# Optimization experiments

Hardware: AMD Instinct MI355X
Metric: run time of the kernel (lower is better)

## Reference

```python
import jax, jax.numpy as jnp
import numpy as np

D = 512        # input_dim
T = 64         # n_trees
DEPTH = 3
NI = 2 ** DEPTH - 1   # 7 internal nodes
NL = 2 ** DEPTH       # 8 leaves
PPT = NI * D + NI + NL * 2   # params per tree
TOT = PPT * T + T            # + tree_weights
HID = 64


def setup_inputs() -> dict:
    key = jax.random.key(0)
    ks = jax.random.split(key, 10)
    w = lambda k, s: jax.random.normal(k, s, jnp.float32) * 0.05  # xavier-ish small gain
    return {
        "X_train": jax.random.normal(ks[0], (8192, D), jnp.float32),
        "X_test": jax.random.normal(ks[1], (32768, D), jnp.float32),
        "y_train": jax.random.randint(ks[2], (8192,), 0, 2, jnp.int64),
        "W1": w(ks[3], (HID, D)), "b1": jnp.zeros(HID), "g1": jnp.ones(HID), "be1": jnp.zeros(HID),
        "W2": w(ks[4], (HID, HID)), "b2": jnp.zeros(HID),
        "H1": w(ks[5], (2 * HID, HID)), "hb1": jnp.zeros(2 * HID),
        "g2": jnp.ones(2 * HID), "be2": jnp.zeros(2 * HID),
        "H2": w(ks[6], (2 * HID, 2 * HID)), "hb2": jnp.zeros(2 * HID),
        "H3": w(ks[7], (TOT, 2 * HID)), "hb3": jnp.zeros(TOT),
    }


def _ln(x, g, b, eps=1e-5):
    m = x.mean(-1, keepdims=True)
    v = ((x - m) ** 2).mean(-1, keepdims=True)
    return (x - m) / jnp.sqrt(v + eps) * g + b


def reference(X_train, X_test, y_train, W1, b1, g1, be1, W2, b2,
              H1, hb1, g2, be2, H2, hb2, H3, hb3):
    # --- hypernet: data encoder + param generator (Dropout is eval=identity) ---
    h = jax.nn.relu(_ln(X_train @ W1.T + b1, g1, be1))
    h = jax.nn.relu(h @ W2.T + b2)
    c = h.mean(axis=0)                              # [HID] context
    u = jax.nn.relu(_ln(c @ H1.T + hb1, g2, be2))
    u = jax.nn.relu(u @ H2.T + hb2)
    params = u @ H3.T + hb3                         # [TOT]

    # --- parse per-tree params (sequential layout) ---
    rows = params[: T * PPT].reshape(T, PPT)
    sw = rows[:, : NI * D].reshape(T, NI, D)        # split weights
    sb = rows[:, NI * D: NI * D + NI]               # split bias [T, NI]
    ll = rows[:, NI * D + NI:].reshape(T, NL, 2)    # leaf logits
    tw = params[T * PPT:]                           # tree weights [T]

    # --- soft decision trees, all trees/nodes batched ---
    # sigmoid split prob for every (sample, tree, internal node); temperature=1
    p = jax.nn.sigmoid(jnp.einsum('bd,tnd->btn', X_test, sw) + sb[None])  # [B,T,NI]
    B = X_test.shape[0]
    lp = jnp.ones((B, T, 1), X_test.dtype)
    for d in range(DEPTH):                          # unrolled fixed-depth traversal
        s = 2 ** d - 1                              # heap offset of level d
        pd = p[:, :, s: s + 2 ** d]                 # [B,T,2^d]
        lp = jnp.stack([lp * (1 - pd), lp * pd], axis=-1).reshape(B, T, 2 ** (d + 1))
    # original code adds leaf contributions twice (main loop + cleanup loop)
    lp = lp * 2.0                                   # [B,T,NL]

    leaf_dist = jax.nn.softmax(ll, axis=-1)         # [T,NL,2]
    out_t = jnp.einsum('btl,tlc->btc', lp, leaf_dist)
    w = jax.nn.softmax(tw, axis=0)                  # [T]
    return jnp.einsum('btc,t->bc', out_t, w)        # [B,2]
```

## Files before the change

kernel.cpp:

```cpp
#include <hip/hip_runtime.h>
#include <hip/hip_bf16.h>

#define DD 512
#define HIDN 64
#define NTREE 64
#define NIN 7
#define PPTC 3607
#define TOTP 230912
#define SWROWS 448

typedef __attribute__((ext_vector_type(8))) short bf16x8;
typedef __attribute__((ext_vector_type(4))) float f32x4;
typedef __attribute__((ext_vector_type(8))) _Float16 h16x8;

__device__ __forceinline__ unsigned short f2bf(float f) {
  unsigned u = __float_as_uint(f);
  unsigned r = (u + 0x7FFFu + ((u >> 16) & 1u)) >> 16;
  return (unsigned short)r;
}
__device__ __forceinline__ float sigmoidf_(float x) {
  return 1.0f / (1.0f + __expf(-x));
}
__device__ __forceinline__ uint2 pack_bf16x4(float4 v) {
  uint2 pk;
  pk.x = (unsigned)f2bf(v.x) | ((unsigned)f2bf(v.y) << 16);
  pk.y = (unsigned)f2bf(v.z) | ((unsigned)f2bf(v.w) << 16);
  return pk;
}

__global__ __launch_bounds__(256) void k_train(
    const float* __restrict__ Xtr, const float* __restrict__ W1,
    const float* __restrict__ b1, const float* __restrict__ g1,
    const float* __restrict__ be1, const float* __restrict__ W2,
    const float* __restrict__ b2, float* __restrict__ c_part)
{
  __shared__ __align__(16) char smem[37888];
  char* Xc  = smem;
  char* W1c = smem + 8192;
  char* Hl  = smem + 24576;
  char* W2l = smem + 28672;
  float* lnb = (float*)(smem + 36864);
  float* cp  = (float*)(smem + 37376);

  const int tid = threadIdx.x;
  const int lane = tid & 63;
  const int wv = tid >> 6;
  const int l15 = lane & 15;
  const int gq = lane >> 4;
  const int wm = wv >> 1;
  const int wn = wv & 1;
  const int rb0 = blockIdx.x * 32;

  const float4* X4g = (const float4*)Xtr;
  const float4* W4g = (const float4*)W1;

#pragma unroll
  for (int s = 0; s < 4; ++s) {
    int fidx = tid + s * 256;
    int n = fidx >> 4, kq = fidx & 15;
    float4 v = ((const float4*)W2)[n * 16 + kq];
    uint2 pk = pack_bf16x4(v);
    int off = n * 128 + kq * 8; off ^= (n & 7) << 4;
    *(uint2*)(W2l + off) = pk;
  }

  int xga[4], xo[4];
#pragma unroll
  for (int s = 0; s < 4; ++s) {
    int f = tid + s * 256;
    int m = f >> 5, kq = f & 31;
    xga[s] = (rb0 + m) * 128 + kq;
    xo[s] = (m * 256 + kq * 8) ^ ((m & 7) << 4);
  }
  int wga[8], wo[8];
#pragma unroll
  for (int s = 0; s < 8; ++s) {
    int f = tid + s * 256;
    int n = f >> 5, kq = f & 31;
    wga[s] = n * 128 + kq;
    wo[s] = (n * 256 + kq * 8) ^ ((n & 7) << 4);
  }

  f32x4 acc1[2];
#pragma unroll
  for (int nt = 0; nt < 2; ++nt) { f32x4 z = {0.f,0.f,0.f,0.f}; acc1[nt] = z; }

  float4 xr[4], wr[8];
#pragma unroll
  for (int s = 0; s < 4; ++s) xr[s] = X4g[xga[s]];
#pragma unroll
  for (int s = 0; s < 8; ++s) wr[s] = W4g[wga[s]];

  for (int kc = 0; kc < 4; ++kc) {
    __syncthreads();
#pragma unroll
    for (int s = 0; s < 4; ++s) *(uint2*)(Xc + xo[s]) = pack_bf16x4(xr[s]);
#pragma unroll
    for (int s = 0; s < 8; ++s) *(uint2*)(W1c + wo[s]) = pack_bf16x4(wr[s]);
    if (kc < 3) {
      int ko = (kc + 1) * 32;
#pragma unroll
      for (int s = 0; s < 4; ++s) xr[s] = X4g[xga[s] + ko];
#pragma unroll
      for (int s = 0; s < 8; ++s) wr[s] = W4g[wga[s] + ko];
    }
    __syncthreads();
#pragma unroll
    for (int ks = 0; ks < 4; ++ks) {
      int arow = wm * 16 + l15;
      int aoff = (arow * 256 + ks * 64 + gq * 16) ^ ((arow & 7) << 4);
      bf16x8 afr = *(const bf16x8*)(Xc + aoff);
#pragma unroll
      for (int nt = 0; nt < 2; ++nt) {
        int brow = wn * 32 + nt * 16 + l15;
        int boff = (brow * 256 + ks * 64 + gq * 16) ^ ((brow & 7) << 4);
        bf16x8 bfr = *(const bf16x8*)(W1c + boff);
        acc1[nt] = __builtin_amdgcn_mfma_f32_16x16x32_bf16(afr, bfr, acc1[nt], 0, 0, 0);
      }
    }
  }

  float b1v[2], g1v[2], be1v[2], b2v[2];
#pragma unroll
  for (int nt = 0; nt < 2; ++nt) {
    int c = wn * 32 + nt * 16 + l15;
    b1v[nt] = b1[c]; g1v[nt] = g1[c]; be1v[nt] = be1[c]; b2v[nt] = b2[c];
  }
  float yv[2][4], s_[4], q_[4];
#pragma unroll
  for (int i = 0; i < 4; ++i) {
    float s = 0.f, q = 0.f;
#pragma unroll
    for (int nt = 0; nt < 2; ++nt) {
      float y = acc1[nt][i] + b1v[nt];
      yv[nt][i] = y; s += y; q += y * y;
    }
    s_[i] = s; q_[i] = q;
  }
#pragma unroll
  for (int off = 1; off < 16; off <<= 1) {
#pragma unroll
    for (int i = 0; i < 4; ++i) {
      s_[i] += __shfl_xor(s_[i], off);
      q_[i] += __shfl_xor(q_[i], off);
    }
  }
  if (l15 == 0) {
#pragma unroll
    for (int i = 0; i < 4; ++i) {
      int row = wm * 16 + gq * 4 + i;
      float2 sv; sv.x = s_[i]; sv.y = q_[i];
      *(float2*)(lnb + (row * 2 + wn) * 2) = sv;
    }
  }
  __syncthreads();
#pragma unroll
  for (int i = 0; i < 4; ++i) {
    int row = wm * 16 + gq * 4 + i;
    float2 e0 = *(float2*)(lnb + (row * 2 + 0) * 2);
    float2 e1 = *(float2*)(lnb + (row * 2 + 1) * 2);
    float m = (e0.x + e1.x) * (1.0f / 64.0f);
    float var = (e0.y + e1.y) * (1.0f / 64.0f) - m * m;
    float rstd = rsqrtf(var + 1e-5f);
#pragma unroll
    for (int nt = 0; nt < 2; ++nt) {
      float h = (yv[nt][i] - m) * rstd * g1v[nt] + be1v[nt];
      h = fmaxf(h, 0.0f);
      int col = wn * 32 + nt * 16 + l15;
      int off2 = (row * 128 + col * 2) ^ ((row & 7) << 4);
      *(unsigned short*)(Hl + off2) = f2bf(h);
    }
  }
  __syncthreads();

  f32x4 acc2[2];
#pragma unroll
  for (int nt = 0; nt < 2; ++nt) { f32x4 z = {0.f,0.f,0.f,0.f}; acc2[nt] = z; }
#pragma unroll
  for (int ks = 0; ks < 2; ++ks) {
    int arow = wm * 16 + l15;
    int aoff = (arow * 128 + ks * 64 + gq * 16) ^ ((arow & 7) << 4);
    bf16x8 afr = *(const bf16x8*)(Hl + aoff);
#pragma unroll
    for (int nt = 0; nt < 2; ++nt) {
      int brow = wn * 32 + nt * 16 + l15;
      int boff = (brow * 128 + ks * 64 + gq * 16) ^ ((brow & 7) << 4);
      bf16x8 bfr = *(const bf16x8*)(W2l + boff);
      acc2[nt] = __builtin_amdgcn_mfma_f32_16x16x32_bf16(afr, bfr, acc2[nt], 0, 0, 0);
    }
  }
  float cs[2];
#pragma unroll
  for (int nt = 0; nt < 2; ++nt) {
    float s = 0.f;
#pragma unroll
    for (int i = 0; i < 4; ++i) s += fmaxf(acc2[nt][i] + b2v[nt], 0.0f);
    cs[nt] = s;
  }
#pragma unroll
  for (int nt = 0; nt < 2; ++nt) {
    cs[nt] += __shfl_xor(cs[nt], 16);
    cs[nt] += __shfl_xor(cs[nt], 32);
  }
  if (lane < 16) {
#pragma unroll
    for (int nt = 0; nt < 2; ++nt)
      cp[wm * 64 + wn * 32 + nt * 16 + lane] = cs[nt];
  }
  __syncthreads();
  if (tid < 64) c_part[blockIdx.x * 64 + tid] = cp[tid] + cp[64 + tid];
}

__global__ __launch_bounds__(128) void k_head(
    const float* __restrict__ c_part,
    const float* __restrict__ H1, const float* __restrict__ hb1,
    const float* __restrict__ g2, const float* __restrict__ be2,
    const float* __restrict__ H2, const float* __restrict__ hb2,
    float* __restrict__ u2out)
{
  __shared__ float clds[64];
  __shared__ float u1lds[128];
  __shared__ float red[4];
  int tid = threadIdx.x;
  if (tid < 64) {
    float s0 = 0.f, s1 = 0.f, s2 = 0.f, s3 = 0.f;
    for (int b = 0; b < 256; b += 4) {
      s0 += c_part[(b + 0) * 64 + tid];
      s1 += c_part[(b + 1) * 64 + tid];
      s2 += c_part[(b + 2) * 64 + tid];
      s3 += c_part[(b + 3) * 64 + tid];
    }
    clds[tid] = (s0 + s1 + s2 + s3) * (1.0f / 8192.0f);
  }
  __syncthreads();
  float a0 = 0.f, a1 = 0.f, a2p = 0.f, a3 = 0.f;
  for (int k = 0; k < 64; k += 4) {
    a0 += clds[k + 0] * H1[tid * 64 + k + 0];
    a1 += clds[k + 1] * H1[tid * 64 + k + 1];
    a2p += clds[k + 2] * H1[tid * 64 + k + 2];
    a3 += clds[k + 3] * H1[tid * 64 + k + 3];
  }
  float acc = hb1[tid] + ((a0 + a1) + (a2p + a3));
  float s = acc, q = acc * acc;
#pragma unroll
  for (int off = 1; off < 64; off <<= 1) { s += __shfl_xor(s, off); q += __shfl_xor(q, off); }
  int wv = tid >> 6;
  if ((tid & 63) == 0) { red[wv * 2] = s; red[wv * 2 + 1] = q; }
  __syncthreads();
  float S = red[0] + red[2], Q = red[1] + red[3];
  float m = S * (1.0f / 128.0f);
  float var = Q * (1.0f / 128.0f) - m * m;
  float rstd = rsqrtf(var + 1e-5f);
  float u1 = fmaxf((acc - m) * rstd * g2[tid] + be2[tid], 0.0f);
  u1lds[tid] = u1;
  __syncthreads();
  float c0 = 0.f, c1 = 0.f, c2 = 0.f, c3 = 0.f;
  for (int k = 0; k < 128; k += 4) {
    c0 += u1lds[k + 0] * H2[tid * 128 + k + 0];
    c1 += u1lds[k + 1] * H2[tid * 128 + k + 1];
    c2 += u1lds[k + 2] * H2[tid * 128 + k + 2];
    c3 += u1lds[k + 3] * H2[tid * 128 + k + 3];
  }
  u2out[tid] = fmaxf(hb2[tid] + ((c0 + c1) + (c2 + c3)), 0.0f);
}

__global__ __launch_bounds__(256) void k_params(
    const float* __restrict__ H3, const float* __restrict__ hb3,
    const float* __restrict__ u2,
    unsigned short* __restrict__ Bsw, float* __restrict__ sb,
    float* __restrict__ ll, float* __restrict__ tw)
{
  __shared__ float u2l[128];
  int tid = threadIdx.x;
  if (tid < 128) u2l[tid] = u2[tid];
  __syncthreads();
  int row = blockIdx.x * 64 + (tid >> 2);
  int sub = tid & 3;
  float acc = 0.0f;
  const float4* H4 = (const float4*)H3;
#pragma unroll
  for (int j = 0; j < 8; ++j) {
    int f = j * 4 + sub;
    float4 v = H4[row * 32 + f];
    acc += v.x * u2l[f * 4] + v.y * u2l[f * 4 + 1] + v.z * u2l[f * 4 + 2] + v.w * u2l[f * 4 + 3];
  }
  acc += __shfl_xor(acc, 1);
  acc += __shfl_xor(acc, 2);
  if (sub == 0) {
    float val = acc + hb3[row];
    if (row >= 230848) {
      tw[row - 230848] = val;
    } else {
      int t = row / PPTC;
      int r = row - t * PPTC;
      if (r < 3584) {
        int n = r >> 9, d = r & 511;
        Bsw[(t * 7 + n) * 512 + d] = f2bf(val);
      } else if (r < 3591) {
        sb[t * 7 + (r - 3584)] = val;
      } else {
        ll[t * 16 + (r - 3591)] = val;
      }
    }
  }
}

__global__ __launch_bounds__(64) void k_qprep(
    const float* __restrict__ ll, const float* __restrict__ tw,
    float* __restrict__ q)
{
  int t = threadIdx.x;
  float x = tw[t];
  float m = x;
#pragma unroll
  for (int off = 1; off < 64; off <<= 1) m = fmaxf(m, __shfl_xor(m, off));
  float e = __expf(x - m);
  float s = e;
#pragma unroll
  for (int off = 1; off < 64; off <<= 1) s += __shfl_xor(s, off);
  float w = e / s;
#pragma unroll
  for (int l = 0; l < 8; ++l) {
    float a = ll[t * 16 + l * 2], b = ll[t * 16 + l * 2 + 1];
    float mm = fmaxf(a, b);
    float e0 = __expf(a - mm), e1 = __expf(b - mm);
    float inv = 2.0f * w / (e0 + e1);
    q[t * 16 + l * 2] = e0 * inv;
    q[t * 16 + l * 2 + 1] = e1 * inv;
  }
}

__global__ __launch_bounds__(512) void k_test(
    const float* __restrict__ Xt, const unsigned short* __restrict__ Bsw,
    const float* __restrict__ sb, const float* __restrict__ q,
    float* __restrict__ out)
{
  __shared__ __align__(16) char smem[76544];
  char* Xb0 = smem;
  char* Xb1 = smem + 8192;
  char* Bb0 = smem + 16384;
  char* Bb1 = smem + 45056;
  char* Pl  = smem + 16384;
  float* sbl  = (float*)(smem + 73728);
  float* outl = (float*)(smem + 75520);

  const int tid = threadIdx.x;
  const int lane = tid & 63;
  const int wv = tid >> 6;
  const int l15 = lane & 15;
  const int gq = lane >> 4;
  const int wm = wv >> 2;
  const int wn = wv & 3;
  const int bm0 = blockIdx.x * 128;
  const bool btail = (tid < 256);

  if (tid < 448) sbl[tid] = sb[tid];

  float qreg[16];
  {
    const float4* q4 = (const float4*)q;
#pragma unroll
    for (int j = 0; j < 4; ++j) {
      float4 v = q4[lane * 4 + j];
      qreg[j * 4] = v.x; qreg[j * 4 + 1] = v.y; qreg[j * 4 + 2] = v.z; qreg[j * 4 + 3] = v.w;
    }
  }

  const int xm = tid >> 3, xk = tid & 7;
  const int xg0 = (bm0 + xm) * 128 + xk;
  const int xg1 = (bm0 + xm + 64) * 128 + xk;
  const int xo0 = (xm * 64 + xk * 8) ^ ((xm & 7) << 4);
  const int xo1 = ((xm + 64) * 64 + xk * 8) ^ ((xm & 7) << 4);

  int bg[4], bo[4];
#pragma unroll
  for (int s = 0; s < 4; ++s) {
    int idx = tid + s * 512;
    int n = idx >> 2, part = idx & 3;
    bg[s] = n * 64 + part;
    bo[s] = (n * 64 + part * 16) ^ ((n & 7) << 4);
  }

  int aoffs[4], boffs[7];
#pragma unroll
  for (int mt = 0; mt < 4; ++mt) {
    int r = wm * 64 + mt * 16 + l15;
    aoffs[mt] = (r * 64 + gq * 16) ^ ((r & 7) << 4);
  }
#pragma unroll
  for (int nt = 0; nt < 7; ++nt) {
    int r = wn * 112 + nt * 16 + l15;
    boffs[nt] = (r * 64 + gq * 16) ^ ((r & 7) << 4);
  }

  f32x4 acc[4][7];
#pragma unroll
  for (int mt = 0; mt < 4; ++mt)
#pragma unroll
    for (int nt = 0; nt < 7; ++nt) { f32x4 z = {0.f,0.f,0.f,0.f}; acc[mt][nt] = z; }

  const float4* X4 = (const float4*)Xt;
  const uint4* B4 = (const uint4*)Bsw;

#define LOADX(xa, xb, kt) do { xa = X4[xg0 + (kt) * 8]; xb = X4[xg1 + (kt) * 8]; } while (0)
#define LOADB(b0_, b1_, b2_, b3_, kt) do { \
    b0_ = B4[bg[0] + (kt) * 4]; b1_ = B4[bg[1] + (kt) * 4]; b2_ = B4[bg[2] + (kt) * 4]; \
    if (btail) b3_ = B4[bg[3] + (kt) * 4]; } while (0)
#define STORET(Xb, Bb, xa, xb, b0_, b1_, b2_, b3_) do { \
    *(uint2*)((Xb) + xo0) = pack_bf16x4(xa); \
    *(uint2*)((Xb) + xo1) = pack_bf16x4(xb); \
    *(uint4*)((Bb) + bo[0]) = b0_; \
    *(uint4*)((Bb) + bo[1]) = b1_; \
    *(uint4*)((Bb) + bo[2]) = b2_; \
    if (btail) *(uint4*)((Bb) + bo[3]) = b3_; } while (0)
#define COMPUTE(Xb, Bb) do { \
    bf16x8 afr[4]; \
    _Pragma("unroll") \
    for (int mt = 0; mt < 4; ++mt) afr[mt] = *(const bf16x8*)((Xb) + aoffs[mt]); \
    _Pragma("unroll") \
    for (int nt = 0; nt < 7; ++nt) { \
      bf16x8 bfr = *(const bf16x8*)((Bb) + boffs[nt]); \
      _Pragma("unroll") \
      for (int mt = 0; mt < 4; ++mt) \
        acc[mt][nt] = __builtin_amdgcn_mfma_f32_16x16x32_bf16(afr[mt], bfr, acc[mt][nt], 0, 0, 0); \
    } } while (0)

  float4 xra, xrb, xca, xcb;
  uint4 ba0, ba1, ba2, ba3, bb0, bb1, bb2, bb3;

  LOADX(xra, xca, 0);
  LOADB(ba0, ba1, ba2, ba3, 0);
  STORET(Xb0, Bb0, xra, xca, ba0, ba1, ba2, ba3);
  LOADX(xrb, xcb, 1);
  LOADB(bb0, bb1, bb2, bb3, 1);
  __syncthreads();

  for (int kt2 = 0; kt2 < 16; kt2 += 2) {
    STORET(Xb1, Bb1, xrb, xcb, bb0, bb1, bb2, bb3);
    if (kt2 + 2 < 16) {
      LOADX(xra, xca, kt2 + 2);
      LOADB(ba0, ba1, ba2, ba3, kt2 + 2);
    }
    COMPUTE(Xb0, Bb0);
    __syncthreads();
    if (kt2 + 2 < 16) {
      STORET(Xb0, Bb0, xra, xca, ba0, ba1, ba2, ba3);
      if (kt2 + 3 < 16) {
        LOADX(xrb, xcb, kt2 + 3);
        LOADB(bb0, bb1, bb2, bb3, kt2 + 3);
      }
    }
    COMPUTE(Xb1, Bb1);
    __syncthreads();
  }

#pragma unroll
  for (int rg = 0; rg < 4; ++rg) {
    if (wm == (rg >> 1)) {
#pragma unroll
      for (int mtl = 0; mtl < 2; ++mtl) {
        const int mt = (rg & 1) * 2 + mtl;
#pragma unroll
        for (int nt = 0; nt < 7; ++nt) {
          int col = wn * 112 + nt * 16 + l15;
          float sbv = sbl[col];
          int t = col / 7;
          int j = col - t * 7;
          int slot2 = (t * 8 + j) * 2;
#pragma unroll
          for (int i = 0; i < 4; ++i) {
            int rl = mtl * 16 + gq * 4 + i;
            float p = sigmoidf_(acc[mt][nt][i] + sbv);
            *(_Float16*)(Pl + rl * 1024 + slot2) = (_Float16)p;
          }
        }
      }
    }
    __syncthreads();
#pragma unroll
    for (int k = 0; k < 4; ++k) {
      int rl = wv * 4 + k;
      h16x8 v = *(const h16x8*)(Pl + rl * 1024 + lane * 16);
      float p0 = (float)v[0], p1 = (float)v[1], p2 = (float)v[2];
      float p3 = (float)v[3], p4 = (float)v[4], p5 = (float)v[5], p6 = (float)v[6];
      float n0 = 1.f - p0, n1 = 1.f - p1, n2 = 1.f - p2;
      float a00 = n0 * n1, a01 = n0 * p1, a10 = p0 * n2, a11 = p0 * p2;
      float L0 = a00 * (1.f - p3), L1 = a00 * p3;
      float L2 = a01 * (1.f - p4), L3 = a01 * p4;
      float L4 = a10 * (1.f - p5), L5 = a10 * p5;
      float L6 = a11 * (1.f - p6), L7 = a11 * p6;
      float o0 = L0*qreg[0] + L1*qreg[2] + L2*qreg[4] + L3*qreg[6]
               + L4*qreg[8] + L5*qreg[10] + L6*qreg[12] + L7*qreg[14];
      float o1 = L0*qreg[1] + L1*qreg[3] + L2*qreg[5] + L3*qreg[7]
               + L4*qreg[9] + L5*qreg[11] + L6*qreg[13] + L7*qreg[15];
#pragma unroll
      for (int off = 1; off < 64; off <<= 1) {
        o0 += __shfl_xor(o0, off);
        o1 += __shfl_xor(o1, off);
      }
      if (lane == 0) {
        int gr = rg * 32 + rl;
        outl[gr * 2] = o0;
        outl[gr * 2 + 1] = o1;
      }
    }
    __syncthreads();
  }
  if (tid < 256) out[bm0 * 2 + tid] = outl[tid];
#undef LOADX
#undef LOADB
#undef STORET
#undef COMPUTE
}

extern "C" void kernel_launch(void* const* d_in, const int* in_sizes, int n_in,
                              void* d_out, int out_size, void* d_ws, size_t ws_size,
                              hipStream_t stream)
{
  const float* Xtr = (const float*)d_in[0];
  const float* Xte = (const float*)d_in[1];
  const float* W1  = (const float*)d_in[3];
  const float* b1  = (const float*)d_in[4];
  const float* g1  = (const float*)d_in[5];
  const float* be1 = (const float*)d_in[6];
  const float* W2  = (const float*)d_in[7];
  const float* b2  = (const float*)d_in[8];
  const float* H1  = (const float*)d_in[9];
  const float* hb1 = (const float*)d_in[10];
  const float* g2  = (const float*)d_in[11];
  const float* be2 = (const float*)d_in[12];
  const float* H2  = (const float*)d_in[13];
  const float* hb2 = (const float*)d_in[14];
  const float* H3  = (const float*)d_in[15];
  const float* hb3 = (const float*)d_in[16];
  float* out = (float*)d_out;
  char* ws = (char*)d_ws;

  float* c_part = (float*)ws;
  float* u2     = (float*)(ws + 65536);
  float* sb     = (float*)(ws + 66048);
  float* ll     = (float*)(ws + 67840);
  float* tw     = (float*)(ws + 71936);
  float* q      = (float*)(ws + 72192);
  unsigned short* Bsw = (unsigned short*)(ws + 76288);

  k_train<<<256, 256, 0, stream>>>(Xtr, W1, b1, g1, be1, W2, b2, c_part);
  k_head<<<1, 128, 0, stream>>>(c_part, H1, hb1, g2, be2, H2, hb2, u2);
  k_params<<<3608, 256, 0, stream>>>(H3, hb3, u2, Bsw, sb, ll, tw);
  k_qprep<<<1, 64, 0, stream>>>(ll, tw, q);
  k_test<<<256, 512, 0, stream>>>(Xte, Bsw, sb, q, out);
}
```

Measured before the change: 84.87 us.

## Fuse leaf-weight prep into test kernel and load X fragments directly to registers

Removes the separate single-block k_qprep launch and computes the tree-weight and leaf softmax inside each k_test block, storing q in LDS. The X tile no longer goes through LDS: each wave loads its own fp32 A fragments from global memory and converts them with packed bf16 conversion instructions, which shrinks shared memory and removes the X stores to LDS. k_head is widened to 256 threads so the partial-context reduction is split four ways. The cost is that every test block repeats the softmax work, and more global X traffic goes straight to registers, where each wave re-reads rows that other waves also read.

```diff
diff --git a/kernel.cpp b/kernel.cpp
--- a/kernel.cpp
+++ b/kernel.cpp
@@ -26,6 +26,16 @@
   pk.x = (unsigned)f2bf(v.x) | ((unsigned)f2bf(v.y) << 16);
   pk.y = (unsigned)f2bf(v.z) | ((unsigned)f2bf(v.w) << 16);
   return pk;
+}
+__device__ __forceinline__ bf16x8 cvt8(float4 a, float4 b) {
+  unsigned u0, u1, u2, u3;
+  asm("v_cvt_pk_bf16_f32 %0, %1, %2" : "=v"(u0) : "v"(a.x), "v"(a.y));
+  asm("v_cvt_pk_bf16_f32 %0, %1, %2" : "=v"(u1) : "v"(a.z), "v"(a.w));
+  asm("v_cvt_pk_bf16_f32 %0, %1, %2" : "=v"(u2) : "v"(b.x), "v"(b.y));
+  asm("v_cvt_pk_bf16_f32 %0, %1, %2" : "=v"(u3) : "v"(b.z), "v"(b.w));
+  union { unsigned u[4]; bf16x8 v; } r;
+  r.u[0] = u0; r.u[1] = u1; r.u[2] = u2; r.u[3] = u3;
+  return r.v;
 }
 
 __global__ __launch_bounds__(256) void k_train(
@@ -211,36 +221,45 @@
   if (tid < 64) c_part[blockIdx.x * 64 + tid] = cp[tid] + cp[64 + tid];
 }
 
-__global__ __launch_bounds__(128) void k_head(
+__global__ __launch_bounds__(256) void k_head(
     const float* __restrict__ c_part,
     const float* __restrict__ H1, const float* __restrict__ hb1,
     const float* __restrict__ g2, const float* __restrict__ be2,
     const float* __restrict__ H2, const float* __restrict__ hb2,
     float* __restrict__ u2out)
 {
+  __shared__ float part[256];
   __shared__ float clds[64];
   __shared__ float u1lds[128];
-  __shared__ float red[4];
+  __shared__ float red[8];
   int tid = threadIdx.x;
-  if (tid < 64) {
+  {
+    int col = tid & 63, g = tid >> 6;
     float s0 = 0.f, s1 = 0.f, s2 = 0.f, s3 = 0.f;
-    for (int b = 0; b < 256; b += 4) {
-      s0 += c_part[(b + 0) * 64 + tid];
-      s1 += c_part[(b + 1) * 64 + tid];
-      s2 += c_part[(b + 2) * 64 + tid];
-      s3 += c_part[(b + 3) * 64 + tid];
-    }
-    clds[tid] = (s0 + s1 + s2 + s3) * (1.0f / 8192.0f);
-  }
-  __syncthreads();
-  float a0 = 0.f, a1 = 0.f, a2p = 0.f, a3 = 0.f;
-  for (int k = 0; k < 64; k += 4) {
-    a0 += clds[k + 0] * H1[tid * 64 + k + 0];
-    a1 += clds[k + 1] * H1[tid * 64 + k + 1];
-    a2p += clds[k + 2] * H1[tid * 64 + k + 2];
-    a3 += clds[k + 3] * H1[tid * 64 + k + 3];
-  }
-  float acc = hb1[tid] + ((a0 + a1) + (a2p + a3));
+    int b0 = g * 64;
+    for (int b = 0; b < 64; b += 4) {
+      s0 += c_part[(b0 + b + 0) * 64 + col];
+      s1 += c_part[(b0 + b + 1) * 64 + col];
+      s2 += c_part[(b0 + b + 2) * 64 + col];
+      s3 += c_part[(b0 + b + 3) * 64 + col];
+    }
+    part[tid] = (s0 + s1) + (s2 + s3);
+  }
+  __syncthreads();
+  if (tid < 64)
+    clds[tid] = (part[tid] + part[64 + tid] + part[128 + tid] + part[192 + tid]) * (1.0f / 8192.0f);
+  __syncthreads();
+  float acc = 0.f;
+  if (tid < 128) {
+    float a0 = 0.f, a1 = 0.f, a2 = 0.f, a3 = 0.f;
+    for (int k = 0; k < 64; k += 4) {
+      a0 += clds[k + 0] * H1[tid * 64 + k + 0];
+      a1 += clds[k + 1] * H1[tid * 64 + k + 1];
+      a2 += clds[k + 2] * H1[tid * 64 + k + 2];
+      a3 += clds[k + 3] * H1[tid * 64 + k + 3];
+    }
+    acc = hb1[tid] + ((a0 + a1) + (a2 + a3));
+  }
   float s = acc, q = acc * acc;
 #pragma unroll
   for (int off = 1; off < 64; off <<= 1) { s += __shfl_xor(s, off); q += __shfl_xor(q, off); }
@@ -251,17 +270,19 @@
   float m = S * (1.0f / 128.0f);
   float var = Q * (1.0f / 128.0f) - m * m;
   float rstd = rsqrtf(var + 1e-5f);
-  float u1 = fmaxf((acc - m) * rstd * g2[tid] + be2[tid], 0.0f);
-  u1lds[tid] = u1;
-  __syncthreads();
-  float c0 = 0.f, c1 = 0.f, c2 = 0.f, c3 = 0.f;
-  for (int k = 0; k < 128; k += 4) {
-    c0 += u1lds[k + 0] * H2[tid * 128 + k + 0];
-    c1 += u1lds[k + 1] * H2[tid * 128 + k + 1];
-    c2 += u1lds[k + 2] * H2[tid * 128 + k + 2];
-    c3 += u1lds[k + 3] * H2[tid * 128 + k + 3];
-  }
-  u2out[tid] = fmaxf(hb2[tid] + ((c0 + c1) + (c2 + c3)), 0.0f);
+  if (tid < 128)
+    u1lds[tid] = fmaxf((acc - m) * rstd * g2[tid] + be2[tid], 0.0f);
+  __syncthreads();
+  if (tid < 128) {
+    float c0 = 0.f, c1 = 0.f, c2 = 0.f, c3 = 0.f;
+    for (int k = 0; k < 128; k += 4) {
+      c0 += u1lds[k + 0] * H2[tid * 128 + k + 0];
+      c1 += u1lds[k + 1] * H2[tid * 128 + k + 1];
+      c2 += u1lds[k + 2] * H2[tid * 128 + k + 2];
+      c3 += u1lds[k + 3] * H2[tid * 128 + k + 3];
+    }
+    u2out[tid] = fmaxf(hb2[tid] + ((c0 + c1) + (c2 + c3)), 0.0f);
+  }
 }
 
 __global__ __launch_bounds__(256) void k_params(
@@ -305,44 +326,18 @@
   }
 }
 
-__global__ __launch_bounds__(64) void k_qprep(
-    const float* __restrict__ ll, const float* __restrict__ tw,
-    float* __restrict__ q)
-{
-  int t = threadIdx.x;
-  float x = tw[t];
-  float m = x;
-#pragma unroll
-  for (int off = 1; off < 64; off <<= 1) m = fmaxf(m, __shfl_xor(m, off));
-  float e = __expf(x - m);
-  float s = e;
-#pragma unroll
-  for (int off = 1; off < 64; off <<= 1) s += __shfl_xor(s, off);
-  float w = e / s;
-#pragma unroll
-  for (int l = 0; l < 8; ++l) {
-    float a = ll[t * 16 + l * 2], b = ll[t * 16 + l * 2 + 1];
-    float mm = fmaxf(a, b);
-    float e0 = __expf(a - mm), e1 = __expf(b - mm);
-    float inv = 2.0f * w / (e0 + e1);
-    q[t * 16 + l * 2] = e0 * inv;
-    q[t * 16 + l * 2 + 1] = e1 * inv;
-  }
-}
-
 __global__ __launch_bounds__(512) void k_test(
     const float* __restrict__ Xt, const unsigned short* __restrict__ Bsw,
-    const float* __restrict__ sb, const float* __restrict__ q,
-    float* __restrict__ out)
+    const float* __restrict__ sb, const float* __restrict__ ll,
+    const float* __restrict__ tw, float* __restrict__ out)
 {
-  __shared__ __align__(16) char smem[76544];
-  char* Xb0 = smem;
-  char* Xb1 = smem + 8192;
-  char* Bb0 = smem + 16384;
-  char* Bb1 = smem + 45056;
-  char* Pl  = smem + 16384;
-  float* sbl  = (float*)(smem + 73728);
-  float* outl = (float*)(smem + 75520);
+  __shared__ __align__(16) char smem[64256];
+  char* Bb0 = smem;
+  char* Bb1 = smem + 28672;
+  char* Pl  = smem;
+  float* qlds = (float*)(smem + 57344);
+  float* sbl  = (float*)(smem + 61440);
+  float* outl = (float*)(smem + 63232);
 
   const int tid = threadIdx.x;
   const int lane = tid & 63;
@@ -354,24 +349,6 @@
   const int bm0 = blockIdx.x * 128;
   const bool btail = (tid < 256);
 
-  if (tid < 448) sbl[tid] = sb[tid];
-
-  float qreg[16];
-  {
-    const float4* q4 = (const float4*)q;
-#pragma unroll
-    for (int j = 0; j < 4; ++j) {
-      float4 v = q4[lane * 4 + j];
-      qreg[j * 4] = v.x; qreg[j * 4 + 1] = v.y; qreg[j * 4 + 2] = v.z; qreg[j * 4 + 3] = v.w;
-    }
-  }
-
-  const int xm = tid >> 3, xk = tid & 7;
-  const int xg0 = (bm0 + xm) * 128 + xk;
-  const int xg1 = (bm0 + xm + 64) * 128 + xk;
-  const int xo0 = (xm * 64 + xk * 8) ^ ((xm & 7) << 4);
-  const int xo1 = ((xm + 64) * 64 + xk * 8) ^ ((xm & 7) << 4);
-
   int bg[4], bo[4];
 #pragma unroll
   for (int s = 0; s < 4; ++s) {
@@ -380,13 +357,13 @@
     bg[s] = n * 64 + part;
     bo[s] = (n * 64 + part * 16) ^ ((n & 7) << 4);
   }
-
-  int aoffs[4], boffs[7];
+  int abase[4];
 #pragma unroll
   for (int mt = 0; mt < 4; ++mt) {
-    int r = wm * 64 + mt * 16 + l15;
-    aoffs[mt] = (r * 64 + gq * 16) ^ ((r & 7) << 4);
-  }
+    int row = bm0 + wm * 64 + mt * 16 + l15;
+    abase[mt] = row * 128 + gq * 2;
+  }
+  int boffs[7];
 #pragma unroll
   for (int nt = 0; nt < 7; ++nt) {
     int r = wn * 112 + nt * 16 + l15;
@@ -402,56 +379,83 @@
   const float4* X4 = (const float4*)Xt;
   const uint4* B4 = (const uint4*)Bsw;
 
-#define LOADX(xa, xb, kt) do { xa = X4[xg0 + (kt) * 8]; xb = X4[xg1 + (kt) * 8]; } while (0)
-#define LOADB(b0_, b1_, b2_, b3_, kt) do { \
-    b0_ = B4[bg[0] + (kt) * 4]; b1_ = B4[bg[1] + (kt) * 4]; b2_ = B4[bg[2] + (kt) * 4]; \
-    if (btail) b3_ = B4[bg[3] + (kt) * 4]; } while (0)
-#define STORET(Xb, Bb, xa, xb, b0_, b1_, b2_, b3_) do { \
-    *(uint2*)((Xb) + xo0) = pack_bf16x4(xa); \
-    *(uint2*)((Xb) + xo1) = pack_bf16x4(xb); \
-    *(uint4*)((Bb) + bo[0]) = b0_; \
-    *(uint4*)((Bb) + bo[1]) = b1_; \
-    *(uint4*)((Bb) + bo[2]) = b2_; \
-    if (btail) *(uint4*)((Bb) + bo[3]) = b3_; } while (0)
-#define COMPUTE(Xb, Bb) do { \
-    bf16x8 afr[4]; \
-    _Pragma("unroll") \
-    for (int mt = 0; mt < 4; ++mt) afr[mt] = *(const bf16x8*)((Xb) + aoffs[mt]); \
-    _Pragma("unroll") \
+  float4 af[4][2];
+  bf16x8 abf[4];
+  uint4 br0, br1, br2, br3;
+
+#define LOADA(kt) do { _Pragma("unroll") \
+    for (int mt = 0; mt < 4; ++mt) { \
+      af[mt][0] = X4[abase[mt] + (kt) * 8]; \
+      af[mt][1] = X4[abase[mt] + (kt) * 8 + 1]; } } while (0)
+#define CVTA() do { _Pragma("unroll") \
+    for (int mt = 0; mt < 4; ++mt) abf[mt] = cvt8(af[mt][0], af[mt][1]); } while (0)
+#define LOADB(kt) do { \
+    br0 = B4[bg[0] + (kt) * 4]; br1 = B4[bg[1] + (kt) * 4]; \
+    br2 = B4[bg[2] + (kt) * 4]; if (btail) br3 = B4[bg[3] + (kt) * 4]; } while (0)
+#define STOREB(Bb) do { \
+    *(uint4*)((Bb) + bo[0]) = br0; *(uint4*)((Bb) + bo[1]) = br1; \
+    *(uint4*)((Bb) + bo[2]) = br2; if (btail) *(uint4*)((Bb) + bo[3]) = br3; } while (0)
+#define COMPUTE(Bb) do { _Pragma("unroll") \
     for (int nt = 0; nt < 7; ++nt) { \
       bf16x8 bfr = *(const bf16x8*)((Bb) + boffs[nt]); \
       _Pragma("unroll") \
       for (int mt = 0; mt < 4; ++mt) \
-        acc[mt][nt] = __builtin_amdgcn_mfma_f32_16x16x32_bf16(afr[mt], bfr, acc[mt][nt], 0, 0, 0); \
+        acc[mt][nt] = __builtin_amdgcn_mfma_f32_16x16x32_bf16(abf[mt], bfr, acc[mt][nt], 0, 0, 0); \
     } } while (0)
 
-  float4 xra, xrb, xca, xcb;
-  uint4 ba0, ba1, ba2, ba3, bb0, bb1, bb2, bb3;
-
-  LOADX(xra, xca, 0);
-  LOADB(ba0, ba1, ba2, ba3, 0);
-  STORET(Xb0, Bb0, xra, xca, ba0, ba1, ba2, ba3);
-  LOADX(xrb, xcb, 1);
-  LOADB(bb0, bb1, bb2, bb3, 1);
+  LOADA(0);
+  LOADB(0);
+  STOREB(Bb0);
+  LOADB(1);
+  if (tid < 448) sbl[tid] = sb[tid];
+  if (tid < 64) {
+    int t = tid;
+    float x = tw[t];
+    float m = x;
+#pragma unroll
+    for (int off = 1; off < 64; off <<= 1) m = fmaxf(m, __shfl_xor(m, off));
+    float e = __expf(x - m);
+    float s = e;
+#pragma unroll
+    for (int off = 1; off < 64; off <<= 1) s += __shfl_xor(s, off);
+    float w = e / s;
+#pragma unroll
+    for (int l = 0; l < 8; ++l) {
+      float a = ll[t * 16 + l * 2], b = ll[t * 16 + l * 2 + 1];
+      float mm = fmaxf(a, b);
+      float e0 = __expf(a - mm), e1 = __expf(b - mm);
+      float inv = 2.0f * w / (e0 + e1);
+      qlds[t * 16 + l * 2] = e0 * inv;
+      qlds[t * 16 + l * 2 + 1] = e1 * inv;
+    }
+  }
   __syncthreads();
 
   for (int kt2 = 0; kt2 < 16; kt2 += 2) {
-    STORET(Xb1, Bb1, xrb, xcb, bb0, bb1, bb2, bb3);
+    CVTA();
+    STOREB(Bb1);
+    if (kt2 + 2 < 16) LOADB(kt2 + 2);
+    LOADA(kt2 + 1);
+    COMPUTE(Bb0);
+    __syncthreads();
+    CVTA();
     if (kt2 + 2 < 16) {
-      LOADX(xra, xca, kt2 + 2);
-      LOADB(ba0, ba1, ba2, ba3, kt2 + 2);
-    }
-    COMPUTE(Xb0, Bb0);
+      STOREB(Bb0);
+      if (kt2 + 3 < 16) LOADB(kt2 + 3);
+      LOADA(kt2 + 2);
+    }
+    COMPUTE(Bb1);
     __syncthreads();
-    if (kt2 + 2 < 16) {
-      STORET(Xb0, Bb0, xra, xca, ba0, ba1, ba2, ba3);
-      if (kt2 + 3 < 16) {
-        LOADX(xrb, xcb, kt2 + 3);
-        LOADB(bb0, bb1, bb2, bb3, kt2 + 3);
-      }
-    }
-    COMPUTE(Xb1, Bb1);
-    __syncthreads();
+  }
+
+  float qreg[16];
+  {
+    const float4* q4 = (const float4*)qlds;
+#pragma unroll
+    for (int j = 0; j < 4; ++j) {
+      float4 v = q4[lane * 4 + j];
+      qreg[j * 4] = v.x; qreg[j * 4 + 1] = v.y; qreg[j * 4 + 2] = v.z; qreg[j * 4 + 3] = v.w;
+    }
   }
 
 #pragma unroll
@@ -507,9 +511,10 @@
     __syncthreads();
   }
   if (tid < 256) out[bm0 * 2 + tid] = outl[tid];
-#undef LOADX
+#undef LOADA
+#undef CVTA
 #undef LOADB
-#undef STORET
+#undef STOREB
 #undef COMPUTE
 }
 
@@ -541,12 +546,10 @@
   float* sb     = (float*)(ws + 66048);
   float* ll     = (float*)(ws + 67840);
   float* tw     = (float*)(ws + 71936);
-  float* q      = (float*)(ws + 72192);
-  unsigned short* Bsw = (unsigned short*)(ws + 76288);
+  unsigned short* Bsw = (unsigned short*)(ws + 72192);
 
   k_train<<<256, 256, 0, stream>>>(Xtr, W1, b1, g1, be1, W2, b2, c_part);
-  k_head<<<1, 128, 0, stream>>>(c_part, H1, hb1, g2, be2, H2, hb2, u2);
+  k_head<<<1, 256, 0, stream>>>(c_part, H1, hb1, g2, be2, H2, hb2, u2);
   k_params<<<3608, 256, 0, stream>>>(H3, hb3, u2, Bsw, sb, ll, tw);
-  k_qprep<<<1, 64, 0, stream>>>(ll, tw, q);
-  k_test<<<256, 512, 0, stream>>>(Xte, Bsw, sb, q, out);
-}
+  k_test<<<256, 512, 0, stream>>>(Xte, Bsw, sb, ll, tw, out);
+}
```

After: 101.3 us. +19.4%, slower.
